# Performance work log

Hardware: AMD Instinct MI355X
Metric: run time of the kernel (lower is better)

The kernel has to match this reference:

```python
import jax, jax.numpy as jnp
import numpy as np

NUM_HEADS = 8
DIM = 384
KSIZE = 9  # res_kernel_size


def _moe_fc(x2d, gate_w, gate_b, w0, b0, w1, b1):
    # NaiveGate with top_k=1: softmax over a single top-1 logit == 1.0, so the
    # SparseDispatcher dispatch/exp/mul/log combine reduces exactly to selecting
    # the argmax expert's output per token.
    logits = x2d @ gate_w + gate_b                      # [T, 2]
    sel = jnp.argmax(logits, axis=-1)[:, None]          # [T, 1]
    y0 = x2d @ w0.T + b0
    y1 = x2d @ w1.T + b1
    return jnp.where(sel == 0, y0, y1)


def _forward(x, qkv_gate_w, qkv_gate_b, qkv_w0, qkv_w1,
             proj_gate_w, proj_gate_b, proj_w0, proj_b0, proj_w1, proj_b1,
             dconv_w):
    B, N, C = x.shape
    h, hd = NUM_HEADS, C // NUM_HEADS
    xt = x.reshape(-1, C)
    zero3 = jnp.zeros((3 * C,), x.dtype)  # qkv_bias=False
    qkv = _moe_fc(xt, qkv_gate_w, qkv_gate_b, qkv_w0, zero3, qkv_w1, zero3)
    qkv = qkv.reshape(B, N, 3, h, hd).transpose(2, 0, 3, 1, 4)  # [3,B,h,N,d]
    q, k, v = qkv[0], qkv[1], qkv[2]

    q = q / jnp.linalg.norm(q, axis=-1, keepdims=True)
    k = k / jnp.linalg.norm(k, axis=-1, keepdims=True)
    scale1 = jnp.mean(jnp.abs(q))
    scale2 = jnp.mean(jnp.abs(k))
    # straight-through binarization: fwd value = (x>0)*scale, grad flows via clamp(x,0,1)
    cq = jnp.clip(q, 0.0, 1.0)
    q = jax.lax.stop_gradient((q > 0).astype(q.dtype) * scale1 - cq) + cq
    ck = jnp.clip(k, 0.0, 1.0)
    k = jax.lax.stop_gradient((k > 0).astype(k.dtype) * scale2 - ck) + ck

    # depthwise residual conv over the token axis: v is [B, h, N, d], kernel (9,1)
    dconv_v = jax.lax.conv_general_dilated(
        v, dconv_w, window_strides=(1, 1), padding=[(KSIZE // 2, KSIZE // 2), (0, 0)],
        feature_group_count=h, dimension_numbers=("NCHW", "OIHW", "NCHW"))

    # linear-attention reorder: (K^T V) first -> O(N d^2)
    attn = jnp.einsum("bhnd,bhne->bhde", k, v)          # [B,h,d,d]
    out = 0.5 * v - (1.0 / jnp.pi) * jnp.einsum("bhnd,bhde->bhne", q, attn)
    out = out / jnp.linalg.norm(out, axis=-1, keepdims=True)
    out = out + dconv_v
    out = out.transpose(0, 2, 1, 3).reshape(B, N, C)

    out = _moe_fc(out.reshape(-1, C), proj_gate_w, proj_gate_b,
                  proj_w0, proj_b0, proj_w1, proj_b1)
    return out.reshape(B, N, C)


def setup_inputs() -> dict:
    key = jax.random.key(0)
    ks = jax.random.split(key, 12)
    B, N, C = 8, 4096, DIM
    s = 0.02
    return {
        "x": jax.random.normal(ks[0], (B, N, C), jnp.float32),
        "H": 64,
        "W": 64,
        "qkv_gate_w": jax.random.normal(ks[1], (C, 2), jnp.float32) * s,
        "qkv_gate_b": jnp.zeros((2,), jnp.float32),
        "qkv_w0": jax.random.normal(ks[2], (3 * C, C), jnp.float32) * s,
        "qkv_w1": jax.random.normal(ks[3], (3 * C, C), jnp.float32) * s,
        "proj_gate_w": jax.random.normal(ks[4], (C, 2), jnp.float32) * s,
        "proj_gate_b": jnp.zeros((2,), jnp.float32),
        "proj_w0": jax.random.normal(ks[5], (C, C), jnp.float32) * s,
        "proj_b0": jnp.zeros((C,), jnp.float32),
        "proj_w1": jax.random.normal(ks[6], (C, C), jnp.float32) * s,
        "proj_b1": jnp.zeros((C,), jnp.float32),
        "dconv_w": jax.random.normal(ks[7], (NUM_HEADS, 1, KSIZE, 1), jnp.float32) * s,
    }


def reference(x, H, W, qkv_gate_w, qkv_gate_b, qkv_w0, qkv_w1,
              proj_gate_w, proj_gate_b, proj_w0, proj_b0, proj_w1, proj_b1,
              dconv_w):
    # H, W are unused by the math (kept for signature fidelity)
    return _forward(x, qkv_gate_w, qkv_gate_b, qkv_w0, qkv_w1,
                    proj_gate_w, proj_gate_b, proj_w0, proj_b0, proj_w1, proj_b1,
                    dconv_w)
```

## Files before the change

kernel.cpp:

```cpp
#include <hip/hip_runtime.h>
#include <hip/hip_bf16.h>

#define BB 8
#define NN 4096
#define CC 384
#define HH 8
#define DD 48
#define TT (BB*NN)
#define CAP (TT + 128)
#define NQ ((size_t)BB*HH*NN*DD)
#define LISTCAP 32768

static_assert(CAP % 128 == 0, "cap");

typedef __attribute__((ext_vector_type(8))) short bf16x8;
typedef __attribute__((ext_vector_type(4))) float f32x4;

__device__ __forceinline__ float waveRedSum(float v){
  #pragma unroll
  for (int o = 32; o > 0; o >>= 1) v += __shfl_xor(v, o);
  return v;
}

__device__ __forceinline__ unsigned short f2bf(float f){
  unsigned u = __float_as_uint(f);
  u += 0x7FFFu + ((u >> 16) & 1u);
  return (unsigned short)(u >> 16);
}
__device__ __forceinline__ float bf2f(unsigned short h){
  return __uint_as_float(((unsigned)h) << 16);
}

__global__ void k_init(int* __restrict__ perm0, int* __restrict__ perm1, int* __restrict__ cur){
  int i = blockIdx.x * 256 + threadIdx.x;
  if (i < 8) cur[i] = 0;
  if (i < CAP){ perm0[i] = -1; perm1[i] = -1; }
}

__global__ void k_cvt_split(const float* __restrict__ src, unsigned short* __restrict__ hi,
                            unsigned short* __restrict__ lo, int n4){
  int i = blockIdx.x*256 + threadIdx.x;
  if (i >= n4) return;
  float4 v = ((const float4*)src)[i];
  float f[4] = {v.x, v.y, v.z, v.w};
  unsigned short h[4], l[4];
  #pragma unroll
  for (int j = 0; j < 4; j++){
    h[j] = f2bf(f[j]);
    l[j] = f2bf(f[j] - bf2f(h[j]));
  }
  uint2 hv, lv;
  hv.x = h[0] | ((unsigned)h[1] << 16); hv.y = h[2] | ((unsigned)h[3] << 16);
  lv.x = l[0] | ((unsigned)l[1] << 16); lv.y = l[2] | ((unsigned)l[3] << 16);
  ((uint2*)hi)[i] = hv;
  ((uint2*)lo)[i] = lv;
}

__global__ void k_cvt_weights(const float* __restrict__ qw0, const float* __restrict__ qw1,
                              const float* __restrict__ pw0, const float* __restrict__ pw1,
                              unsigned short* __restrict__ qw0h, unsigned short* __restrict__ qw0l,
                              unsigned short* __restrict__ qw1h, unsigned short* __restrict__ qw1l,
                              unsigned short* __restrict__ pw0h, unsigned short* __restrict__ pw0l,
                              unsigned short* __restrict__ pw1h, unsigned short* __restrict__ pw1l){
  const int NQW = 1152*384/4, NPW = 384*384/4;
  int i = blockIdx.x*256 + threadIdx.x;
  const float* src; unsigned short* hi; unsigned short* lo; int off;
  if (i < NQW){ src = qw0; hi = qw0h; lo = qw0l; off = i; }
  else if (i < 2*NQW){ src = qw1; hi = qw1h; lo = qw1l; off = i - NQW; }
  else if (i < 2*NQW + NPW){ src = pw0; hi = pw0h; lo = pw0l; off = i - 2*NQW; }
  else if (i < 2*NQW + 2*NPW){ src = pw1; hi = pw1h; lo = pw1l; off = i - 2*NQW - NPW; }
  else return;
  float4 v = ((const float4*)src)[off];
  float f[4] = {v.x, v.y, v.z, v.w};
  unsigned short h[4], l[4];
  #pragma unroll
  for (int j = 0; j < 4; j++){
    h[j] = f2bf(f[j]);
    l[j] = f2bf(f[j] - bf2f(h[j]));
  }
  uint2 hv, lv;
  hv.x = h[0] | ((unsigned)h[1] << 16); hv.y = h[2] | ((unsigned)h[3] << 16);
  lv.x = l[0] | ((unsigned)l[1] << 16); lv.y = l[2] | ((unsigned)l[3] << 16);
  ((uint2*)hi)[off] = hv;
  ((uint2*)lo)[off] = lv;
}

__global__ void k_gate_scatter(const float* __restrict__ X,
                               const float* __restrict__ gw, const float* __restrict__ gb,
                               int* __restrict__ perm, int* __restrict__ cur,
                               unsigned char* __restrict__ selb){
  const int lane = threadIdx.x & 63;
  const int wave = threadIdx.x >> 6;
  float gd[6];
  #pragma unroll
  for (int j = 0; j < 6; j++){
    int c = lane + 64*j;
    gd[j] = gw[c*2+1] - gw[c*2];
  }
  const float gbd = gb[1] - gb[0];
  const int tok0 = (blockIdx.x*4 + wave) * 8;
  unsigned mask = 0u;
  for (int i = 0; i < 8; i++){
    const float* xr = X + (size_t)(tok0 + i) * CC;
    float d = 0.f;
    #pragma unroll
    for (int j = 0; j < 6; j++) d = fmaf(xr[lane + 64*j], gd[j], d);
    d = waveRedSum(d);
    if (d + gbd > 0.f) mask |= (1u << i);
  }
  int n1 = __popc(mask), n0 = 8 - n1;
  int b0 = 0, b1 = 0;
  if (lane == 0){
    b0 = atomicAdd(cur + 0, n0);
    b1 = atomicAdd(cur + 1, n1);
  }
  b0 = __shfl(b0, 0); b1 = __shfl(b1, 0);
  if (lane < 8){
    int sel = (mask >> lane) & 1;
    unsigned below = mask & ((1u << lane) - 1u);
    int r1 = __popc(below);
    int r0 = lane - r1;
    int idx = sel ? (CAP - 1 - (b1 + r1)) : (b0 + r0);
    perm[idx] = tok0 + lane;
    selb[tok0 + lane] = (unsigned char)sel;
  }
}

__global__ void k_gate2(const float* __restrict__ gpart, const float* __restrict__ gb,
                        int* __restrict__ perm, int* __restrict__ cur){
  const int t = blockIdx.x*256 + threadIdx.x;
  const int lane = threadIdx.x & 63;
  const float gbd = gb[1] - gb[0];
  float4 a = ((const float4*)(gpart + (size_t)t*8))[0];
  float4 c = ((const float4*)(gpart + (size_t)t*8))[1];
  float d = ((a.x + a.y) + (a.z + a.w)) + ((c.x + c.y) + (c.z + c.w)) + gbd;
  bool sel = d > 0.f;
  unsigned long long m = __ballot(sel);
  int n1 = (int)__popcll(m);
  int b0 = 0, b1 = 0;
  if (lane == 0){
    b0 = atomicAdd(cur + 0, 64 - n1);
    b1 = atomicAdd(cur + 1, n1);
  }
  b0 = __shfl(b0, 0); b1 = __shfl(b1, 0);
  unsigned long long below = m & ((1ull << lane) - 1ull);
  int r1 = (int)__popcll(below);
  int r0 = lane - r1;
  int idx = sel ? (CAP - 1 - (b1 + r1)) : (b0 + r0);
  perm[idx] = t;
}

template<int NCOLS, int PASSES, bool IS_QKV>
__global__ __launch_bounds__(256, 2)
void k_gemm_mfma(const unsigned short* __restrict__ Ahi_g, const unsigned short* __restrict__ Alo_g,
                 const unsigned short* __restrict__ W0h, const unsigned short* __restrict__ W0l,
                 const unsigned short* __restrict__ W1h, const unsigned short* __restrict__ W1l,
                 const float* __restrict__ bias0, const float* __restrict__ bias1,
                 const int* __restrict__ perm, const int* __restrict__ cur,
                 unsigned short* __restrict__ oq, unsigned short* __restrict__ ok,
                 float* __restrict__ ov, float* __restrict__ oproj,
                 int* __restrict__ tlist, int* __restrict__ tcnt)
{
  constexpr int GDX = NCOLS / 128;
  constexpr int NWG = GDX * (CAP/128);
  constexpr int NB = (PASSES == 3) ? 2 : 1;
  __shared__ unsigned short As[2][NB][128*32];
  __shared__ unsigned short Bs[2][NB][128*32];
  __shared__ int permv[128];

  int orig = blockIdx.y * GDX + blockIdx.x;
  constexpr int qq = NWG >> 3, rr = NWG & 7;
  int xcd = orig & 7, slot = orig >> 3;
  int logical = (xcd < rr) ? (xcd*(qq+1) + slot) : (rr*(qq+1) + (xcd-rr)*qq + slot);
  const int bx = logical % GDX, by = logical / GDX;

  const int tid = threadIdx.x;
  const int m0 = by * 128, n0 = bx * 128;
  if (tid < 128) permv[tid] = perm[m0 + tid];
  __syncthreads();
  const int expert = (m0 > cur[0]) ? 1 : 0;
  const unsigned short* Wh = expert ? W1h : W0h;
  const unsigned short* Wl = expert ? W1l : W0l;

  const int c0 = tid, c1 = tid + 256;
  const int r0 = c0 >> 2, r1 = c1 >> 2;
  const int s0 = (((c0 & 3) ^ ((r0 >> 1) & 3))) * 8;
  const int s1 = (((c1 & 3) ^ ((r1 >> 1) & 3))) * 8;
  int t0 = permv[r0]; if (t0 < 0) t0 = 0;
  int t1 = permv[r1]; if (t1 < 0) t1 = 0;
  const unsigned short* a0h = Ahi_g + (size_t)t0*CC + s0;
  const unsigned short* a1h = Ahi_g + (size_t)t1*CC + s1;
  const unsigned short* b0h = Wh + (size_t)(n0 + r0)*CC + s0;
  const unsigned short* b1h = Wh + (size_t)(n0 + r1)*CC + s1;
  const unsigned short* a0l = nullptr; const unsigned short* a1l = nullptr;
  const unsigned short* b0l = nullptr; const unsigned short* b1l = nullptr;
  if constexpr (PASSES == 3){
    a0l = Alo_g + (size_t)t0*CC + s0;
    a1l = Alo_g + (size_t)t1*CC + s1;
    b0l = Wl + (size_t)(n0 + r0)*CC + s0;
    b1l = Wl + (size_t)(n0 + r1)*CC + s1;
  }
  const int d0 = c0*8, d1 = c1*8;

  const int lane = tid & 63;
  const int wv = tid >> 6, wr = wv >> 1, wc2 = wv & 1;
  const int lr = lane & 15, lg = lane >> 4;

  f32x4 acc[4][4];
  #pragma unroll
  for (int i = 0; i < 4; i++)
    #pragma unroll
    for (int j = 0; j < 4; j++) acc[i][j] = (f32x4){0.f, 0.f, 0.f, 0.f};

  int aoff[4], boff[4];
  #pragma unroll
  for (int f = 0; f < 4; f++){
    int ra = wr*64 + f*16 + lr;
    aoff[f] = ra*32 + ((lg ^ ((ra >> 1) & 3)) * 8);
    int rb = wc2*64 + f*16 + lr;
    boff[f] = rb*32 + ((lg ^ ((rb >> 1) & 3)) * 8);
  }

  #define GLD(gp, lp) __builtin_amdgcn_global_load_lds( \
      (const __attribute__((address_space(1))) void*)(gp), \
      (__attribute__((address_space(3))) void*)(lp), 16, 0, 0)

  #define STAGE(bi, KO) do { \
    GLD(a0h + (KO), &As[bi][0][d0]); \
    GLD(a1h + (KO), &As[bi][0][d1]); \
    GLD(b0h + (KO), &Bs[bi][0][d0]); \
    GLD(b1h + (KO), &Bs[bi][0][d1]); \
    if constexpr (PASSES == 3){ \
      GLD(a0l + (KO), &As[bi][1][d0]); \
      GLD(a1l + (KO), &As[bi][1][d1]); \
      GLD(b0l + (KO), &Bs[bi][1][d0]); \
      GLD(b1l + (KO), &Bs[bi][1][d1]); \
    } \
  } while(0)

  STAGE(0, 0);
  __syncthreads();
  for (int ko = 0; ko < CC; ko += 32){
    const int cb = (ko >> 5) & 1;
    if (ko + 32 < CC) STAGE(cb ^ 1, ko + 32);
    bf16x8 ah[4], bh[4], al[4], bl[4];
    #pragma unroll
    for (int f = 0; f < 4; f++){
      ah[f] = *(const bf16x8*)&As[cb][0][aoff[f]];
      bh[f] = *(const bf16x8*)&Bs[cb][0][boff[f]];
      if constexpr (PASSES == 3){
        al[f] = *(const bf16x8*)&As[cb][1][aoff[f]];
        bl[f] = *(const bf16x8*)&Bs[cb][1][boff[f]];
      }
    }
    #pragma unroll
    for (int mf = 0; mf < 4; mf++)
      #pragma unroll
      for (int nf = 0; nf < 4; nf++){
        acc[mf][nf] = __builtin_amdgcn_mfma_f32_16x16x32_bf16(ah[mf], bh[nf], acc[mf][nf], 0, 0, 0);
        if constexpr (PASSES == 3){
          acc[mf][nf] = __builtin_amdgcn_mfma_f32_16x16x32_bf16(al[mf], bh[nf], acc[mf][nf], 0, 0, 0);
          acc[mf][nf] = __builtin_amdgcn_mfma_f32_16x16x32_bf16(ah[mf], bl[nf], acc[mf][nf], 0, 0, 0);
        }
      }
    __syncthreads();
  }
  #undef STAGE
  #undef GLD

  #pragma unroll
  for (int mf = 0; mf < 4; mf++){
    #pragma unroll
    for (int j = 0; j < 4; j++){
      const int rl = wr*64 + mf*16 + lg*4 + j;
      const int t = permv[rl];
      if (t < 0) continue;
      const int b = t >> 12, nn = t & 4095;
      #pragma unroll
      for (int nf = 0; nf < 4; nf++){
        const int col = n0 + wc2*64 + nf*16 + lr;
        const float val = acc[mf][nf][j];
        if constexpr (IS_QKV){
          const int which = col / CC;
          const int rem = col - which*CC;
          const int h = rem / DD;
          const int e = rem - h*DD;
          const size_t off = (((size_t)b*HH + h)*NN + nn)*DD + e;
          if (which == 0){
            oq[off] = f2bf(val);
            if (fabsf(val) < 2.5e-5f){
              int pq = atomicAdd(tcnt, 1);
              if (pq < LISTCAP) tlist[pq] = (int)off;
            }
          } else if (which == 1){
            ok[off] = f2bf(val);
            if (fabsf(val) < 2.5e-5f){
              int pq = atomicAdd(tcnt, 1);
              if (pq < LISTCAP) tlist[pq] = (int)(off + NQ);
            }
          } else {
            ov[off] = val;
          }
        } else {
          const float* bs = expert ? bias1 : bias0;
          oproj[(size_t)t*CC + col] = val + bs[col];
        }
      }
    }
  }
}

__global__ void k_topup_fix(unsigned short* __restrict__ qb, unsigned short* __restrict__ kb,
                            const int* __restrict__ list, const int* __restrict__ cnt,
                            const float* __restrict__ x,
                            const float* __restrict__ w0, const float* __restrict__ w1,
                            const unsigned char* __restrict__ selb){
  const int lane = threadIdx.x & 63;
  const int gw = (blockIdx.x*256 + threadIdx.x) >> 6;
  const int nwaves = gridDim.x * 4;
  int n = cnt[0]; if (n > LISTCAP) n = LISTCAP;
  for (int e = gw; e < n; e += nwaves){
    int idx = list[e];
    int isK = (idx >= (int)NQ);
    int li = isK ? idx - (int)NQ : idx;
    int d = li % DD; int rest = li / DD;
    int nn = rest & 4095; int bh = rest >> 12;
    int b = bh >> 3, h = bh & 7;
    int t = b*NN + nn;
    int col = (isK ? CC : 0) + h*DD + d;
    const float* w = selb[t] ? w1 : w0;
    const float* xr = x + (size_t)t*CC;
    const float* wr = w + (size_t)col*CC;
    float s = 0.f;
    #pragma unroll
    for (int j = 0; j < 6; j++) s = fmaf(xr[lane + 64*j], wr[lane + 64*j], s);
    s = waveRedSum(s);
    if (lane == 0) (isK ? kb : qb)[li] = f2bf(s);
  }
}

__global__ void k_scales(const unsigned short* __restrict__ qb, const unsigned short* __restrict__ kb,
                         float* __restrict__ part){
  __shared__ float sq[256], sk[256];
  const int row = blockIdx.x*256 + threadIdx.x;
  const uint4* qp = (const uint4*)(qb + (size_t)row*DD);
  const uint4* kp = (const uint4*)(kb + (size_t)row*DD);
  float qss = 0.f, qsa = 0.f, kss = 0.f, ksa = 0.f;
  #pragma unroll
  for (int j = 0; j < 6; j++){
    uint4 u = qp[j];
    unsigned w[4] = {u.x, u.y, u.z, u.w};
    #pragma unroll
    for (int q2 = 0; q2 < 4; q2++){
      float f0 = bf2f((unsigned short)(w[q2] & 0xFFFFu));
      float f1 = bf2f((unsigned short)(w[q2] >> 16));
      qss = fmaf(f0, f0, qss); qsa += fabsf(f0);
      qss = fmaf(f1, f1, qss); qsa += fabsf(f1);
    }
    uint4 v = kp[j];
    unsigned w2[4] = {v.x, v.y, v.z, v.w};
    #pragma unroll
    for (int q2 = 0; q2 < 4; q2++){
      float f0 = bf2f((unsigned short)(w2[q2] & 0xFFFFu));
      float f1 = bf2f((unsigned short)(w2[q2] >> 16));
      kss = fmaf(f0, f0, kss); ksa += fabsf(f0);
      kss = fmaf(f1, f1, kss); ksa += fabsf(f1);
    }
  }
  sq[threadIdx.x] = qsa / sqrtf(qss);
  sk[threadIdx.x] = ksa / sqrtf(kss);
  __syncthreads();
  for (int s = 128; s > 0; s >>= 1){
    if (threadIdx.x < s){ sq[threadIdx.x] += sq[threadIdx.x+s]; sk[threadIdx.x] += sk[threadIdx.x+s]; }
    __syncthreads();
  }
  if (threadIdx.x == 0){
    part[blockIdx.x*2+0] = sq[0];
    part[blockIdx.x*2+1] = sk[0];
  }
}

__global__ void k_attn_partial(const unsigned short* __restrict__ kb, const float* __restrict__ vb,
                               float* __restrict__ part){
  __shared__ float ks[64][48];
  __shared__ float vs[64][48];
  const int bh = blockIdx.x, seg = blockIdx.y;
  const int tid = threadIdx.x;
  const int ti = tid >> 5;
  const int tj = (tid >> 2) & 7;
  const int sl = tid & 3;
  const int dd0 = ti*6, ee0 = tj*6;
  const unsigned short* kbase = kb + ((size_t)bh*NN + seg*512) * DD;
  const float* vbase = vb + ((size_t)bh*NN + seg*512) * DD;
  float acc[6][6] = {};
  for (int c = 0; c < 8; c++){
    __syncthreads();
    for (int f = tid*2; f < 3072; f += 512){
      unsigned kk2 = *(const unsigned*)(kbase + c*3072 + f);
      float2 vv2 = *(const float2*)(vbase + c*3072 + f);
      (&ks[0][0])[f]   = ((short)(unsigned short)(kk2 & 0xFFFFu) > 0) ? 1.f : 0.f;
      (&ks[0][0])[f+1] = ((short)(unsigned short)(kk2 >> 16) > 0) ? 1.f : 0.f;
      (&vs[0][0])[f]   = vv2.x;
      (&vs[0][0])[f+1] = vv2.y;
    }
    __syncthreads();
    for (int nl = sl*16; nl < sl*16 + 16; nl++){
      float kk[6], vv[6];
      #pragma unroll
      for (int i = 0; i < 6; i++){ kk[i] = ks[nl][dd0+i]; vv[i] = vs[nl][ee0+i]; }
      #pragma unroll
      for (int i = 0; i < 6; i++)
        #pragma unroll
        for (int j = 0; j < 6; j++)
          acc[i][j] = fmaf(kk[i], vv[j], acc[i][j]);
    }
  }
  float* p = part + ((size_t)seg*64 + bh) * (DD*DD);
  #pragma unroll
  for (int i = 0; i < 6; i++)
    #pragma unroll
    for (int j = 0; j < 6; j++){
      float a = acc[i][j];
      a += __shfl_xor(a, 1);
      a += __shfl_xor(a, 2);
      if (sl == 0) p[(dd0+i)*48 + (ee0+j)] = a;
    }
}

__global__ void k_attn_reduce(const float* __restrict__ part, const float* __restrict__ scale_part,
                              unsigned short* __restrict__ aTh, unsigned short* __restrict__ aTl,
                              float* __restrict__ scalesb){
  __shared__ float sq[256], sk[256];
  const int t = threadIdx.x;
  float aq = 0.f, ak = 0.f;
  for (int i = t; i < 1024; i += 256){ aq += scale_part[2*i]; ak += scale_part[2*i+1]; }
  sq[t] = aq; sk[t] = ak;
  __syncthreads();
  for (int s = 128; s > 0; s >>= 1){
    if (t < s){ sq[t] += sq[t+s]; sk[t] += sk[t+s]; }
    __syncthreads();
  }
  const float s2 = sk[0] * (1.0f/12582912.0f);
  if (blockIdx.x == 0 && t == 0){
    scalesb[0] = sq[0] * (1.0f/12582912.0f);
    scalesb[1] = s2;
  }
  const int bh = blockIdx.x;
  for (int f = t; f < 3072; f += 256){
    const int e = f >> 6, d = f & 63;
    float s = 0.f;
    if (d < 48){
      #pragma unroll
      for (int seg = 0; seg < 8; seg++) s += part[((size_t)seg*64 + bh)*2304 + d*48 + e];
      s *= s2;
    }
    unsigned short hi = f2bf(s);
    aTh[(size_t)bh*3072 + f] = hi;
    aTl[(size_t)bh*3072 + f] = f2bf(s - bf2f(hi));
  }
}

__global__ __launch_bounds__(256, 4)
void k_fused(const unsigned short* __restrict__ qb, const float* __restrict__ vb,
             const unsigned short* __restrict__ aTh, const unsigned short* __restrict__ aTl,
             const float* __restrict__ scalesb, const float* __restrict__ dw,
             const float* __restrict__ pgw,
             unsigned short* __restrict__ intermh, float* __restrict__ gpart){
  __shared__ unsigned short aT[2][48*72];
  __shared__ float S_lds[128*48];
  __shared__ float wc[16];
  const int chunk = blockIdx.x;
  const int bh = blockIdx.y;
  const int b = bh >> 3, h = bh & 7;
  const int tid = threadIdx.x;
  const int lane = tid & 63, w = tid >> 6;
  const int lr = lane & 15, lg = lane >> 4;

  for (int idx = tid; idx < 384; idx += 256){
    const int e = idx >> 3, sl = idx & 7;
    *(uint4*)&aT[0][e*72 + sl*8] = *(const uint4*)(aTh + (size_t)bh*3072 + e*64 + sl*8);
    *(uint4*)&aT[1][e*72 + sl*8] = *(const uint4*)(aTl + (size_t)bh*3072 + e*64 + sl*8);
  }
  if (tid < 9) wc[tid] = dw[h*9 + tid];
  __syncthreads();

  bf16x8 afr[2][2];
  #pragma unroll
  for (int m = 0; m < 2; m++){
    #pragma unroll
    for (int ks = 0; ks < 2; ks++){
      const int d0 = ks*32 + lg*8;
      bf16x8 a = (bf16x8){0,0,0,0,0,0,0,0};
      if (d0 < 48){
        const int tok = chunk*128 + (w*2+m)*16 + lr;
        uint4 raw = *(const uint4*)(qb + ((size_t)bh*NN + tok)*DD + d0);
        unsigned wd[4] = {raw.x, raw.y, raw.z, raw.w};
        #pragma unroll
        for (int i2 = 0; i2 < 8; i2++){
          unsigned short el = (unsigned short)((wd[i2 >> 1] >> ((i2 & 1)*16)) & 0xFFFFu);
          a[i2] = ((short)el > 0) ? (short)0x3F80 : (short)0;
        }
      }
      afr[m][ks] = a;
    }
  }
  f32x4 acc[2][3];
  #pragma unroll
  for (int m = 0; m < 2; m++)
    #pragma unroll
    for (int nf = 0; nf < 3; nf++) acc[m][nf] = (f32x4){0.f,0.f,0.f,0.f};
  #pragma unroll
  for (int nf = 0; nf < 3; nf++){
    bf16x8 bhv[2], blv[2];
    #pragma unroll
    for (int ks = 0; ks < 2; ks++){
      const int bo = (nf*16 + lr)*72 + ks*32 + lg*8;
      bhv[ks] = *(const bf16x8*)&aT[0][bo];
      blv[ks] = *(const bf16x8*)&aT[1][bo];
    }
    #pragma unroll
    for (int m = 0; m < 2; m++)
      #pragma unroll
      for (int ks = 0; ks < 2; ks++){
        acc[m][nf] = __builtin_amdgcn_mfma_f32_16x16x32_bf16(afr[m][ks], bhv[ks], acc[m][nf], 0, 0, 0);
        acc[m][nf] = __builtin_amdgcn_mfma_f32_16x16x32_bf16(afr[m][ks], blv[ks], acc[m][nf], 0, 0, 0);
      }
  }
  #pragma unroll
  for (int m = 0; m < 2; m++)
    #pragma unroll
    for (int nf = 0; nf < 3; nf++)
      #pragma unroll
      for (int j = 0; j < 4; j++)
        S_lds[((w*2+m)*16 + lg*4 + j)*48 + nf*16 + lr] = acc[m][nf][j];
  __syncthreads();

  const float coef = scalesb[0] * 0.31830988618379067f;
  const float gdh = (lane < 48) ? (pgw[(h*48+lane)*2+1] - pgw[(h*48+lane)*2]) : 0.f;
  const float* vrow = vb + (size_t)bh*NN*DD;
  const int n0 = chunk*128 + w*32;
  float ring[9];
  #pragma unroll
  for (int k2 = 0; k2 < 8; k2++){
    int nn2 = n0 - 4 + k2;
    ring[k2] = (nn2 >= 0 && nn2 < NN && lane < 48) ? vrow[(size_t)nn2*DD + lane] : 0.f;
  }
  for (int it = 0; it < 32; it++){
    const int n = n0 + it;
    const int nh = n + 4;
    ring[8] = (nh < NN && lane < 48) ? vrow[(size_t)nh*DD + lane] : 0.f;
    const float vv = ring[4];
    const float Sv = (lane < 48) ? S_lds[(w*32 + it)*48 + lane] : 0.f;
    float op = 0.5f*vv - coef*Sv;
    float ss = waveRedSum(op*op);
    float res = op / sqrtf(ss);
    float dc = 0.f;
    #pragma unroll
    for (int k2 = 0; k2 < 9; k2++) dc = fmaf(wc[k2], ring[k2], dc);
    float r = res + dc;
    if (lane < 48)
      intermh[((size_t)b*NN + n)*CC + h*DD + lane] = f2bf(r);
    float gp = waveRedSum(r*gdh);
    if (lane == 0) gpart[((size_t)b*NN + n)*8 + h] = gp;
    #pragma unroll
    for (int k2 = 0; k2 < 8; k2++) ring[k2] = ring[k2+1];
  }
}

extern "C" void kernel_launch(void* const* d_in, const int* in_sizes, int n_in,
                              void* d_out, int out_size, void* d_ws, size_t ws_size,
                              hipStream_t stream){
  const float* x    = (const float*)d_in[0];
  const float* qgw  = (const float*)d_in[3];
  const float* qgb  = (const float*)d_in[4];
  const float* qw0  = (const float*)d_in[5];
  const float* qw1  = (const float*)d_in[6];
  const float* pgw  = (const float*)d_in[7];
  const float* pgb  = (const float*)d_in[8];
  const float* pw0  = (const float*)d_in[9];
  const float* pb0  = (const float*)d_in[10];
  const float* pw1  = (const float*)d_in[11];
  const float* pb1  = (const float*)d_in[12];
  const float* dw   = (const float*)d_in[13];
  float* out = (float*)d_out;

  char* p = (char*)d_ws;
  auto alloc = [&](size_t bytes){ char* r = p; p += (bytes + 255) & ~(size_t)255; return r; };

  unsigned short* qbuf = (unsigned short*)alloc(2*NQ);
  unsigned short* kbuf = (unsigned short*)alloc(2*NQ);
  float* vbuf          = (float*)alloc(4*NQ);
  char* xreg           = alloc(4*NQ);
  unsigned short* Xhi  = (unsigned short*)xreg;
  unsigned short* Xlo  = Xhi + NQ;
  unsigned short* intermh = (unsigned short*)xreg;
  unsigned short* qw0h = (unsigned short*)alloc(2*1152*384);
  unsigned short* qw0l = (unsigned short*)alloc(2*1152*384);
  unsigned short* qw1h = (unsigned short*)alloc(2*1152*384);
  unsigned short* qw1l = (unsigned short*)alloc(2*1152*384);
  unsigned short* pw0h = (unsigned short*)alloc(2*384*384);
  unsigned short* pw0l = (unsigned short*)alloc(2*384*384);
  unsigned short* pw1h = (unsigned short*)alloc(2*384*384);
  unsigned short* pw1l = (unsigned short*)alloc(2*384*384);
  float* attn_part     = (float*)alloc(4*(size_t)8*64*2304);
  unsigned short* aTh  = (unsigned short*)alloc(2*(size_t)64*3072);
  unsigned short* aTl  = (unsigned short*)alloc(2*(size_t)64*3072);
  float* scale_part    = (float*)alloc(4*2048);
  float* scalesb       = (float*)alloc(64);
  float* gpart         = (float*)alloc(4*(size_t)TT*8);
  int* perm_qkv        = (int*)alloc(4*CAP);
  int* perm_proj       = (int*)alloc(4*CAP);
  int* cur             = (int*)alloc(64);
  int* list            = (int*)alloc(4*LISTCAP);
  unsigned char* selq  = (unsigned char*)alloc(TT);

  k_init<<<(CAP + 255)/256, 256, 0, stream>>>(perm_qkv, perm_proj, cur);

  k_cvt_split<<<(int)(NQ/4 + 255)/256, 256, 0, stream>>>(x, Xhi, Xlo, (int)(NQ/4));
  k_cvt_weights<<<1152, 256, 0, stream>>>(qw0, qw1, pw0, pw1,
                                          qw0h, qw0l, qw1h, qw1l,
                                          pw0h, pw0l, pw1h, pw1l);

  k_gate_scatter<<<1024, 256, 0, stream>>>(x, qgw, qgb, perm_qkv, cur, selq);

  {
    dim3 g(9, CAP/128);
    k_gemm_mfma<1152, 3, true><<<g, 256, 0, stream>>>(
        Xhi, Xlo, qw0h, qw0l, qw1h, qw1l, nullptr, nullptr,
        perm_qkv, cur, qbuf, kbuf, vbuf, nullptr, list, cur + 4);
  }

  k_topup_fix<<<64, 256, 0, stream>>>(qbuf, kbuf, list, cur + 4, x, qw0, qw1, selq);

  k_scales<<<1024, 256, 0, stream>>>(qbuf, kbuf, scale_part);

  {
    dim3 g(64, 8);
    k_attn_partial<<<g, 256, 0, stream>>>(kbuf, vbuf, attn_part);
  }
  k_attn_reduce<<<64, 256, 0, stream>>>(attn_part, scale_part, aTh, aTl, scalesb);

  {
    dim3 g(32, 64);
    k_fused<<<g, 256, 0, stream>>>(qbuf, vbuf, aTh, aTl, scalesb, dw, pgw, intermh, gpart);
  }

  k_gate2<<<TT/256, 256, 0, stream>>>(gpart, pgb, perm_proj, cur + 2);

  {
    dim3 g(3, CAP/128);
    k_gemm_mfma<384, 1, false><<<g, 256, 0, stream>>>(
        intermh, nullptr, pw0h, pw0l, pw1h, pw1l, pb0, pb1,
        perm_proj, cur + 2, nullptr, nullptr, nullptr, out, nullptr, nullptr);
  }
}
```

Baseline: 449.7 us.

## Fuse input bf16 split into gate kernel and retile MoE GEMM to 128x64

Removes the standalone x hi/lo conversion kernel and writes the split bf16 copies from the gate-scatter kernel while it already reads x, saving one full pass over the input. The MoE GEMM moves from 256-thread 128x128 tiles with double-buffered LDS to 128-thread 128x64 tiles with single-buffered LDS and a sync after each load. This shrinks LDS and register pressure so more blocks can be resident, and reorders the three split-precision MFMA passes. In exchange the kernel gives up its software prefetch overlap, and the gate kernel's hi/lo stores are scalar 2-byte writes.

```diff
diff --git a/kernel.cpp b/kernel.cpp
--- a/kernel.cpp
+++ b/kernel.cpp
@@ -35,25 +35,6 @@
   int i = blockIdx.x * 256 + threadIdx.x;
   if (i < 8) cur[i] = 0;
   if (i < CAP){ perm0[i] = -1; perm1[i] = -1; }
-}
-
-__global__ void k_cvt_split(const float* __restrict__ src, unsigned short* __restrict__ hi,
-                            unsigned short* __restrict__ lo, int n4){
-  int i = blockIdx.x*256 + threadIdx.x;
-  if (i >= n4) return;
-  float4 v = ((const float4*)src)[i];
-  float f[4] = {v.x, v.y, v.z, v.w};
-  unsigned short h[4], l[4];
-  #pragma unroll
-  for (int j = 0; j < 4; j++){
-    h[j] = f2bf(f[j]);
-    l[j] = f2bf(f[j] - bf2f(h[j]));
-  }
-  uint2 hv, lv;
-  hv.x = h[0] | ((unsigned)h[1] << 16); hv.y = h[2] | ((unsigned)h[3] << 16);
-  lv.x = l[0] | ((unsigned)l[1] << 16); lv.y = l[2] | ((unsigned)l[3] << 16);
-  ((uint2*)hi)[i] = hv;
-  ((uint2*)lo)[i] = lv;
 }
 
 __global__ void k_cvt_weights(const float* __restrict__ qw0, const float* __restrict__ qw1,
@@ -88,7 +69,8 @@
 __global__ void k_gate_scatter(const float* __restrict__ X,
                                const float* __restrict__ gw, const float* __restrict__ gb,
                                int* __restrict__ perm, int* __restrict__ cur,
-                               unsigned char* __restrict__ selb){
+                               unsigned char* __restrict__ selb,
+                               unsigned short* __restrict__ Xhi, unsigned short* __restrict__ Xlo){
   const int lane = threadIdx.x & 63;
   const int wave = threadIdx.x >> 6;
   float gd[6];
@@ -101,10 +83,17 @@
   const int tok0 = (blockIdx.x*4 + wave) * 8;
   unsigned mask = 0u;
   for (int i = 0; i < 8; i++){
-    const float* xr = X + (size_t)(tok0 + i) * CC;
+    const size_t rowoff = (size_t)(tok0 + i) * CC;
+    const float* xr = X + rowoff;
     float d = 0.f;
     #pragma unroll
-    for (int j = 0; j < 6; j++) d = fmaf(xr[lane + 64*j], gd[j], d);
+    for (int j = 0; j < 6; j++){
+      float xv = xr[lane + 64*j];
+      d = fmaf(xv, gd[j], d);
+      unsigned short h = f2bf(xv);
+      Xhi[rowoff + lane + 64*j] = h;
+      Xlo[rowoff + lane + 64*j] = f2bf(xv - bf2f(h));
+    }
     d = waveRedSum(d);
     if (d + gbd > 0.f) mask |= (1u << i);
   }
@@ -151,7 +140,7 @@
 }
 
 template<int NCOLS, int PASSES, bool IS_QKV>
-__global__ __launch_bounds__(256, 2)
+__global__ __launch_bounds__(128)
 void k_gemm_mfma(const unsigned short* __restrict__ Ahi_g, const unsigned short* __restrict__ Alo_g,
                  const unsigned short* __restrict__ W0h, const unsigned short* __restrict__ W0l,
                  const unsigned short* __restrict__ W1h, const unsigned short* __restrict__ W1l,
@@ -161,11 +150,11 @@
                  float* __restrict__ ov, float* __restrict__ oproj,
                  int* __restrict__ tlist, int* __restrict__ tcnt)
 {
-  constexpr int GDX = NCOLS / 128;
+  constexpr int GDX = NCOLS / 64;
   constexpr int NWG = GDX * (CAP/128);
   constexpr int NB = (PASSES == 3) ? 2 : 1;
-  __shared__ unsigned short As[2][NB][128*32];
-  __shared__ unsigned short Bs[2][NB][128*32];
+  __shared__ unsigned short As[NB][128*32];
+  __shared__ unsigned short Bs[NB][64*32];
   __shared__ int permv[128];
 
   int orig = blockIdx.y * GDX + blockIdx.x;
@@ -175,35 +164,38 @@
   const int bx = logical % GDX, by = logical / GDX;
 
   const int tid = threadIdx.x;
-  const int m0 = by * 128, n0 = bx * 128;
-  if (tid < 128) permv[tid] = perm[m0 + tid];
+  const int m0 = by * 128, n0 = bx * 64;
+  permv[tid] = perm[m0 + tid];
   __syncthreads();
   const int expert = (m0 > cur[0]) ? 1 : 0;
   const unsigned short* Wh = expert ? W1h : W0h;
   const unsigned short* Wl = expert ? W1l : W0l;
 
-  const int c0 = tid, c1 = tid + 256;
-  const int r0 = c0 >> 2, r1 = c1 >> 2;
-  const int s0 = (((c0 & 3) ^ ((r0 >> 1) & 3))) * 8;
-  const int s1 = (((c1 & 3) ^ ((r1 >> 1) & 3))) * 8;
-  int t0 = permv[r0]; if (t0 < 0) t0 = 0;
-  int t1 = permv[r1]; if (t1 < 0) t1 = 0;
-  const unsigned short* a0h = Ahi_g + (size_t)t0*CC + s0;
-  const unsigned short* a1h = Ahi_g + (size_t)t1*CC + s1;
-  const unsigned short* b0h = Wh + (size_t)(n0 + r0)*CC + s0;
-  const unsigned short* b1h = Wh + (size_t)(n0 + r1)*CC + s1;
-  const unsigned short* a0l = nullptr; const unsigned short* a1l = nullptr;
-  const unsigned short* b0l = nullptr; const unsigned short* b1l = nullptr;
-  if constexpr (PASSES == 3){
-    a0l = Alo_g + (size_t)t0*CC + s0;
-    a1l = Alo_g + (size_t)t1*CC + s1;
-    b0l = Wl + (size_t)(n0 + r0)*CC + s0;
-    b1l = Wl + (size_t)(n0 + r1)*CC + s1;
-  }
-  const int d0 = c0*8, d1 = c1*8;
-
-  const int lane = tid & 63;
-  const int wv = tid >> 6, wr = wv >> 1, wc2 = wv & 1;
+  const unsigned short* aph[4]; const unsigned short* apl[4];
+  int da[4];
+  #pragma unroll
+  for (int i = 0; i < 4; i++){
+    const int c = tid + 128*i;
+    const int r = c >> 2;
+    const int s = (((c & 3) ^ ((r >> 1) & 3))) * 8;
+    int t = permv[r]; if (t < 0) t = 0;
+    aph[i] = Ahi_g + (size_t)t*CC + s;
+    if (PASSES == 3) apl[i] = Alo_g + (size_t)t*CC + s;
+    da[i] = c*8;
+  }
+  const unsigned short* bph[2]; const unsigned short* bpl[2];
+  int db[2];
+  #pragma unroll
+  for (int i = 0; i < 2; i++){
+    const int c = tid + 128*i;
+    const int r = c >> 2;
+    const int s = (((c & 3) ^ ((r >> 1) & 3))) * 8;
+    bph[i] = Wh + (size_t)(n0 + r)*CC + s;
+    if (PASSES == 3) bpl[i] = Wl + (size_t)(n0 + r)*CC + s;
+    db[i] = c*8;
+  }
+
+  const int lane = tid & 63, w = tid >> 6;
   const int lr = lane & 15, lg = lane >> 4;
 
   f32x4 acc[4][4];
@@ -215,9 +207,9 @@
   int aoff[4], boff[4];
   #pragma unroll
   for (int f = 0; f < 4; f++){
-    int ra = wr*64 + f*16 + lr;
+    int ra = w*64 + f*16 + lr;
     aoff[f] = ra*32 + ((lg ^ ((ra >> 1) & 3)) * 8);
-    int rb = wc2*64 + f*16 + lr;
+    int rb = f*16 + lr;
     boff[f] = rb*32 + ((lg ^ ((rb >> 1) & 3)) * 8);
   }
 
@@ -225,60 +217,64 @@
       (const __attribute__((address_space(1))) void*)(gp), \
       (__attribute__((address_space(3))) void*)(lp), 16, 0, 0)
 
-  #define STAGE(bi, KO) do { \
-    GLD(a0h + (KO), &As[bi][0][d0]); \
-    GLD(a1h + (KO), &As[bi][0][d1]); \
-    GLD(b0h + (KO), &Bs[bi][0][d0]); \
-    GLD(b1h + (KO), &Bs[bi][0][d1]); \
-    if constexpr (PASSES == 3){ \
-      GLD(a0l + (KO), &As[bi][1][d0]); \
-      GLD(a1l + (KO), &As[bi][1][d1]); \
-      GLD(b0l + (KO), &Bs[bi][1][d0]); \
-      GLD(b1l + (KO), &Bs[bi][1][d1]); \
-    } \
-  } while(0)
-
-  STAGE(0, 0);
-  __syncthreads();
   for (int ko = 0; ko < CC; ko += 32){
-    const int cb = (ko >> 5) & 1;
-    if (ko + 32 < CC) STAGE(cb ^ 1, ko + 32);
-    bf16x8 ah[4], bh[4], al[4], bl[4];
-    #pragma unroll
-    for (int f = 0; f < 4; f++){
-      ah[f] = *(const bf16x8*)&As[cb][0][aoff[f]];
-      bh[f] = *(const bf16x8*)&Bs[cb][0][boff[f]];
+    #pragma unroll
+    for (int i = 0; i < 4; i++){
+      GLD(aph[i] + ko, &As[0][da[i]]);
+      if constexpr (PASSES == 3) GLD(apl[i] + ko, &As[1][da[i]]);
+    }
+    #pragma unroll
+    for (int i = 0; i < 2; i++){
+      GLD(bph[i] + ko, &Bs[0][db[i]]);
+      if constexpr (PASSES == 3) GLD(bpl[i] + ko, &Bs[1][db[i]]);
+    }
+    __syncthreads();
+    {
+      bf16x8 ah[4], bh[4];
+      #pragma unroll
+      for (int f = 0; f < 4; f++){
+        ah[f] = *(const bf16x8*)&As[0][aoff[f]];
+        bh[f] = *(const bf16x8*)&Bs[0][boff[f]];
+      }
+      #pragma unroll
+      for (int mf = 0; mf < 4; mf++)
+        #pragma unroll
+        for (int nf = 0; nf < 4; nf++)
+          acc[mf][nf] = __builtin_amdgcn_mfma_f32_16x16x32_bf16(ah[mf], bh[nf], acc[mf][nf], 0, 0, 0);
       if constexpr (PASSES == 3){
-        al[f] = *(const bf16x8*)&As[cb][1][aoff[f]];
-        bl[f] = *(const bf16x8*)&Bs[cb][1][boff[f]];
+        bf16x8 bl[4];
+        #pragma unroll
+        for (int f = 0; f < 4; f++) bl[f] = *(const bf16x8*)&Bs[1][boff[f]];
+        #pragma unroll
+        for (int mf = 0; mf < 4; mf++)
+          #pragma unroll
+          for (int nf = 0; nf < 4; nf++)
+            acc[mf][nf] = __builtin_amdgcn_mfma_f32_16x16x32_bf16(ah[mf], bl[nf], acc[mf][nf], 0, 0, 0);
+        bf16x8 al[4];
+        #pragma unroll
+        for (int f = 0; f < 4; f++) al[f] = *(const bf16x8*)&As[1][aoff[f]];
+        #pragma unroll
+        for (int mf = 0; mf < 4; mf++)
+          #pragma unroll
+          for (int nf = 0; nf < 4; nf++)
+            acc[mf][nf] = __builtin_amdgcn_mfma_f32_16x16x32_bf16(al[mf], bh[nf], acc[mf][nf], 0, 0, 0);
       }
     }
-    #pragma unroll
-    for (int mf = 0; mf < 4; mf++)
-      #pragma unroll
-      for (int nf = 0; nf < 4; nf++){
-        acc[mf][nf] = __builtin_amdgcn_mfma_f32_16x16x32_bf16(ah[mf], bh[nf], acc[mf][nf], 0, 0, 0);
-        if constexpr (PASSES == 3){
-          acc[mf][nf] = __builtin_amdgcn_mfma_f32_16x16x32_bf16(al[mf], bh[nf], acc[mf][nf], 0, 0, 0);
-          acc[mf][nf] = __builtin_amdgcn_mfma_f32_16x16x32_bf16(ah[mf], bl[nf], acc[mf][nf], 0, 0, 0);
-        }
-      }
     __syncthreads();
   }
-  #undef STAGE
   #undef GLD
 
   #pragma unroll
   for (int mf = 0; mf < 4; mf++){
     #pragma unroll
     for (int j = 0; j < 4; j++){
-      const int rl = wr*64 + mf*16 + lg*4 + j;
+      const int rl = w*64 + mf*16 + lg*4 + j;
       const int t = permv[rl];
       if (t < 0) continue;
       const int b = t >> 12, nn = t & 4095;
       #pragma unroll
       for (int nf = 0; nf < 4; nf++){
-        const int col = n0 + wc2*64 + nf*16 + lr;
+        const int col = n0 + nf*16 + lr;
         const float val = acc[mf][nf][j];
         if constexpr (IS_QKV){
           const int which = col / CC;
@@ -616,16 +612,15 @@
 
   k_init<<<(CAP + 255)/256, 256, 0, stream>>>(perm_qkv, perm_proj, cur);
 
-  k_cvt_split<<<(int)(NQ/4 + 255)/256, 256, 0, stream>>>(x, Xhi, Xlo, (int)(NQ/4));
   k_cvt_weights<<<1152, 256, 0, stream>>>(qw0, qw1, pw0, pw1,
                                           qw0h, qw0l, qw1h, qw1l,
                                           pw0h, pw0l, pw1h, pw1l);
 
-  k_gate_scatter<<<1024, 256, 0, stream>>>(x, qgw, qgb, perm_qkv, cur, selq);
+  k_gate_scatter<<<1024, 256, 0, stream>>>(x, qgw, qgb, perm_qkv, cur, selq, Xhi, Xlo);
 
   {
-    dim3 g(9, CAP/128);
-    k_gemm_mfma<1152, 3, true><<<g, 256, 0, stream>>>(
+    dim3 g(1152/64, CAP/128);
+    k_gemm_mfma<1152, 3, true><<<g, 128, 0, stream>>>(
         Xhi, Xlo, qw0h, qw0l, qw1h, qw1l, nullptr, nullptr,
         perm_qkv, cur, qbuf, kbuf, vbuf, nullptr, list, cur + 4);
   }
@@ -648,8 +643,8 @@
   k_gate2<<<TT/256, 256, 0, stream>>>(gpart, pgb, perm_proj, cur + 2);
 
   {
-    dim3 g(3, CAP/128);
-    k_gemm_mfma<384, 1, false><<<g, 256, 0, stream>>>(
+    dim3 g(384/64, CAP/128);
+    k_gemm_mfma<384, 1, false><<<g, 128, 0, stream>>>(
         intermh, nullptr, pw0h, pw0l, pw1h, pw1l, pb0, pb1,
         perm_proj, cur + 2, nullptr, nullptr, nullptr, out, nullptr, nullptr);
   }
```

New measurement: 461.2 us. 1.03x slower.
